# Optimization experiments

Hardware: AMD Instinct MI355X
Metric: run time of the kernel (lower is better)

## Reference

```python
import jax, jax.numpy as jnp
import numpy as np

T, D_IN, D_INT, D_OUT, B = 4096, 256, 256, 256, 8


def setup_inputs() -> dict:
    key = jax.random.key(0)
    ks = jax.random.split(key, 12)
    s_in = 1.0 / np.sqrt(D_IN)
    s_int = 1.0 / np.sqrt(D_INT)
    return {
        "x_batched": jax.random.normal(ks[0], (B, 1, T, D_IN), dtype=jnp.float32),
        "d_gamma_batched": jax.random.uniform(ks[1], (T, T), dtype=jnp.float32),
        "Wq": jax.random.uniform(ks[2], (D_IN, D_INT), jnp.float32, -s_in, s_in),
        "bq": jax.random.uniform(ks[3], (D_INT,), jnp.float32, -s_in, s_in),
        "Wk": jax.random.uniform(ks[4], (D_IN, D_INT), jnp.float32, -s_in, s_in),
        "bk": jax.random.uniform(ks[5], (D_INT,), jnp.float32, -s_in, s_in),
        "Wv": jax.random.uniform(ks[6], (D_IN, D_INT), jnp.float32, -s_in, s_in),
        "bv": jax.random.uniform(ks[7], (D_INT,), jnp.float32, -s_in, s_in),
        "Wo": jax.random.uniform(ks[8], (D_INT, D_OUT), jnp.float32, -s_int, s_int),
        "bo": jax.random.uniform(ks[9], (D_OUT,), jnp.float32, -s_int, s_int),
        "prelu_a": jnp.float32(0.25),  # PReLU single shared parameter, torch default init
    }


def reference(x_batched, d_gamma_batched, Wq, bq, Wk, bk, Wv, bv, Wo, bo, prelu_a):
    # x_batched: [B, 1, T, D_in] -> per-sample [T, D_in]
    x = x_batched.reshape(x_batched.shape[0], T, D_IN)  # [B, T, D_in]
    q = x @ Wq + bq  # [B, T, D_int]
    k = x @ Wk + bk
    v = x @ Wv + bv
    scores = jnp.einsum('btd,bsd->bts', q, k)  # [B, T, T] QK^T per sample
    retained = jnp.einsum('bts,bsd->btd', d_gamma_batched * scores, v)  # decay-gated, matmul V
    y = retained @ Wo + bo  # [B, T, D_out]
    out = jnp.where(y >= 0, y, prelu_a * y)  # PReLU
    return out  # [B, num_nodes=T, D_out]
```

## Files before the change

kernel.cpp:

```cpp
#include <hip/hip_runtime.h>

typedef unsigned short u16;
typedef __bf16 bf16x8 __attribute__((ext_vector_type(8)));
typedef float f32x4 __attribute__((ext_vector_type(4)));
typedef u16 u16x8 __attribute__((ext_vector_type(8)));

constexpr int T_DIM = 4096;
constexpr int DH    = 256;

__device__ __forceinline__ u16 f2bf(float f) {
    union { float f; unsigned u; } v; v.f = f;
    return (u16)((v.u + 0x7FFFu + ((v.u >> 16) & 1u)) >> 16);
}

__device__ __forceinline__ void gload_lds(const void* g, void* l) {
    __builtin_amdgcn_global_load_lds(
        (const __attribute__((address_space(1))) void*)g,
        (__attribute__((address_space(3))) void*)l, 16, 0, 0);
}

__global__ __launch_bounds__(256) void prep_w(
    const float* __restrict__ Wq, const float* __restrict__ Wk,
    const float* __restrict__ Wv, const float* __restrict__ Wo,
    u16* __restrict__ Wqt, u16* __restrict__ Wkt,
    u16* __restrict__ Wvt, u16* __restrict__ Wot)
{
    int idx = blockIdx.x * 256 + threadIdx.x;
    int j = idx >> 8, k = idx & 255;
    int s = k * 256 + j;
    Wqt[idx] = f2bf(Wq[s]);
    Wkt[idx] = f2bf(Wk[s]);
    Wvt[idx] = f2bf(Wv[s]);
    Wot[idx] = f2bf(Wo[s]);
}

__global__ __launch_bounds__(512, 2) void qkv_kernel(
    const float* __restrict__ x,
    const u16* __restrict__ Wqt, const u16* __restrict__ Wkt, const u16* __restrict__ Wvt,
    const float* __restrict__ bq, const float* __restrict__ bk, const float* __restrict__ bv,
    u16* __restrict__ Qg, u16* __restrict__ Kg, u16* __restrict__ Vtg)
{
    __shared__ __align__(16) char lds[131072];
    char* xl = lds;
    const int tid = threadIdx.x;
    const int w = tid >> 6, l = tid & 63;
    const int lr = l & 15, lh = l >> 4;
    const long row0 = (long)blockIdx.x * 128;
    const long bb   = row0 >> 12;
    const int  t0   = (int)(row0 & 4095);

    const u16*  Wt3[3] = { Wqt, Wkt, Wvt };
    const float* b3[3] = { bq, bk, bv };

    {
        char* wb = lds + 65536;
        const char* ws = (const char*)Wqt;
        #pragma unroll
        for (int i = 0; i < 4; ++i) {
            int off = tid * 16 + i * 8192;
            int roww = off >> 9, slot = (off >> 4) & 31;
            gload_lds(ws + roww * 512 + ((slot * 16) ^ ((roww & 7) << 4)), wb + off);
        }
    }
    #pragma unroll
    for (int i = 0; i < 8; ++i) {
        int sid = tid + i * 512;
        int row = sid >> 5, slot = sid & 31;
        const float* src = x + (row0 + row) * DH + slot * 8;
        float4 a  = *(const float4*)(src);
        float4 b2 = *(const float4*)(src + 4);
        u16x8 p;
        p[0] = f2bf(a.x);  p[1] = f2bf(a.y);  p[2] = f2bf(a.z);  p[3] = f2bf(a.w);
        p[4] = f2bf(b2.x); p[5] = f2bf(b2.y); p[6] = f2bf(b2.z); p[7] = f2bf(b2.w);
        *(u16x8*)(xl + row * 512 + ((slot * 16) ^ ((row & 7) << 4))) = p;
    }
    __syncthreads();

    bf16x8 af[8];
    const int arow = w * 16 + lr;
    #pragma unroll
    for (int ks = 0; ks < 8; ++ks)
        af[ks] = *(const bf16x8*)(xl + arow * 512 + ((ks * 64 + lh * 16) ^ ((arow & 7) << 4)));

    for (int p = 0; p < 12; ++p) {
        char* wb = lds + 65536 + (p & 1) * 32768;
        if (p < 11) {
            int pn = p + 1;
            const char* ws = (const char*)Wt3[pn >> 2] + (pn & 3) * 32768;
            char* wn = lds + 65536 + (pn & 1) * 32768;
            #pragma unroll
            for (int i = 0; i < 4; ++i) {
                int off = tid * 16 + i * 8192;
                int roww = off >> 9, slot = (off >> 4) & 31;
                gload_lds(ws + roww * 512 + ((slot * 16) ^ ((roww & 7) << 4)), wn + off);
            }
        }
        const int tgt = p >> 2, qtr = p & 3;
        f32x4 acc[4] = {};
        #pragma unroll
        for (int ks = 0; ks < 8; ++ks) {
            #pragma unroll
            for (int n = 0; n < 4; ++n) {
                int nl = n * 16 + lr;
                bf16x8 bf = *(const bf16x8*)(wb + nl * 512 + ((ks * 64 + lh * 16) ^ ((nl & 7) << 4)));
                acc[n] = __builtin_amdgcn_mfma_f32_16x16x32_bf16(af[ks], bf, acc[n], 0, 0, 0);
            }
        }
        const float* bias = b3[tgt];
        if (tgt < 2) {
            u16* dst = (tgt == 0) ? Qg : Kg;
            long grow = row0 + w * 16 + lh * 4;
            #pragma unroll
            for (int n = 0; n < 4; ++n) {
                int col = qtr * 64 + n * 16 + lr;
                float bbv = bias[col];
                #pragma unroll
                for (int r = 0; r < 4; ++r)
                    dst[(grow + r) * DH + col] = f2bf(acc[n][r] + bbv);
            }
        } else {
            #pragma unroll
            for (int n = 0; n < 4; ++n) {
                int d = qtr * 64 + n * 16 + lr;
                float bbv = bias[d];
                #pragma unroll
                for (int r = 0; r < 4; ++r) {
                    int t = w * 16 + lh * 4 + r;
                    *(u16*)(xl + d * 256 + ((t * 2) ^ ((d & 7) << 4))) = f2bf(acc[n][r] + bbv);
                }
            }
        }
        __syncthreads();
    }

    #pragma unroll
    for (int i = 0; i < 8; ++i) {
        int sid = tid + i * 512;
        int d = sid >> 4, slot = sid & 15;
        u16x8 v = *(const u16x8*)(xl + d * 256 + ((slot * 16) ^ ((d & 7) << 4)));
        *(u16x8*)((char*)Vtg + ((bb * DH + d) * T_DIM + t0) * 2 + slot * 16) = v;
    }
}

__global__ __launch_bounds__(512, 2) void retention_kernel(
    const u16* __restrict__ Qg, const u16* __restrict__ Kg, const u16* __restrict__ Vtg,
    const float* __restrict__ gamma, const u16* __restrict__ Wot,
    const float* __restrict__ bo, const float* __restrict__ pa,
    float* __restrict__ out)
{
    __shared__ __align__(16) char base[147456];
    char* pl = base + 131072;
    const int tid = threadIdx.x;
    const int w = tid >> 6, l = tid & 63;
    const int lr = l & 15, lh = l >> 4;
    const int wq = w >> 1, dh = w & 1;
    const int b  = blockIdx.x >> 5;
    const int q0 = (blockIdx.x & 31) * 128;

    const char* kgb = (const char*)(Kg + (long)b * T_DIM * DH);
    const char* vgb = (const char*)Vtg + (long)b * DH * T_DIM * 2;
    const float* gwave = gamma + (long)(q0 + wq * 32) * T_DIM + dh * 32;

    bf16x8 qf[2][8];
    #pragma unroll
    for (int rg = 0; rg < 2; ++rg) {
        const char* qb = (const char*)(Qg + ((long)b * T_DIM + q0 + wq * 32 + rg * 16 + lr) * DH);
        #pragma unroll
        for (int ks = 0; ks < 8; ++ks)
            qf[rg][ks] = *(const bf16x8*)(qb + ks * 64 + lh * 16);
    }

    f32x4 acc[2][8] = {};

    {
        char* kn = base;
        #pragma unroll
        for (int i = 0; i < 4; ++i) {
            int off = w * 4096 + i * 1024 + l * 16;
            int row = off >> 9, slot = (off >> 4) & 31;
            gload_lds(kgb + row * 512 + ((slot * 16) ^ ((row & 7) << 4)),
                      kn + w * 4096 + i * 1024);
        }
        char* vn = base + 32768;
        #pragma unroll
        for (int i = 0; i < 4; ++i) {
            int off = w * 4096 + i * 1024 + l * 16;
            int row = off >> 7, slot = (off >> 4) & 7;
            gload_lds(vgb + (long)row * (T_DIM * 2) + ((slot * 16) ^ ((row & 7) << 4)),
                      vn + w * 4096 + i * 1024);
        }
    }

    for (int it = 0; it < 64; ++it) {
        const int s0 = it * 64;
        char* kl = base + (it & 1) * 65536;
        char* vl = kl + 32768;

        float gv0[2][4], gv1[2][4];
        {
            const float* gp = gwave + s0;
            #pragma unroll
            for (int n = 0; n < 2; ++n)
                #pragma unroll
                for (int r = 0; r < 4; ++r) {
                    gv0[n][r] = gp[(long)(lh * 4 + r) * T_DIM + n * 16 + lr];
                    gv1[n][r] = gp[(long)(16 + lh * 4 + r) * T_DIM + n * 16 + lr];
                }
        }
        __builtin_amdgcn_sched_barrier(0);

        asm volatile("s_waitcnt vmcnt(16)" ::: "memory");
        __builtin_amdgcn_s_barrier();
        __builtin_amdgcn_sched_barrier(0);

        if (it < 63) {
            const char* kg = kgb + (long)(s0 + 64) * 512;
            char* kn = base + ((it + 1) & 1) * 65536;
            #pragma unroll
            for (int i = 0; i < 4; ++i) {
                int off = w * 4096 + i * 1024 + l * 16;
                int row = off >> 9, slot = (off >> 4) & 31;
                gload_lds(kg + row * 512 + ((slot * 16) ^ ((row & 7) << 4)),
                          kn + w * 4096 + i * 1024);
            }
            const char* vg = vgb + (long)(s0 + 64) * 2;
            char* vn = kn + 32768;
            #pragma unroll
            for (int i = 0; i < 4; ++i) {
                int off = w * 4096 + i * 1024 + l * 16;
                int row = off >> 7, slot = (off >> 4) & 7;
                gload_lds(vg + (long)row * (T_DIM * 2) + ((slot * 16) ^ ((row & 7) << 4)),
                          vn + w * 4096 + i * 1024);
            }
        }

        #pragma unroll
        for (int n = 0; n < 2; ++n) {
            f32x4 sa = {}, sb = {};
            const int srow = dh * 32 + n * 16 + lr;
            #pragma unroll
            for (int ks = 0; ks < 8; ++ks) {
                bf16x8 kf = *(const bf16x8*)(kl + srow * 512 + ((ks * 64 + lh * 16) ^ ((srow & 7) << 4)));
                sa = __builtin_amdgcn_mfma_f32_16x16x32_bf16(qf[0][ks], kf, sa, 0, 0, 0);
                sb = __builtin_amdgcn_mfma_f32_16x16x32_bf16(qf[1][ks], kf, sb, 0, 0, 0);
            }
            const int cb = (dh * 32 + n * 16 + lr) * 2;
            #pragma unroll
            for (int r = 0; r < 4; ++r) {
                int pr0 = wq * 32 + lh * 4 + r;
                int pr1 = pr0 + 16;
                *(__bf16*)(pl + pr0 * 128 + (cb ^ (((pr0 >> 1) & 7) << 4))) =
                    (__bf16)(gv0[n][r] * sa[r]);
                *(__bf16*)(pl + pr1 * 128 + (cb ^ (((pr1 >> 1) & 7) << 4))) =
                    (__bf16)(gv1[n][r] * sb[r]);
            }
        }

        __builtin_amdgcn_sched_barrier(0);
        asm volatile("s_waitcnt lgkmcnt(0)" ::: "memory");
        __builtin_amdgcn_s_barrier();
        __builtin_amdgcn_sched_barrier(0);

        bf16x8 pa2[2][2];
        #pragma unroll
        for (int rg = 0; rg < 2; ++rg)
            #pragma unroll
            for (int k2 = 0; k2 < 2; ++k2) {
                int prr = wq * 32 + rg * 16 + lr;
                pa2[rg][k2] = *(const bf16x8*)(pl + prr * 128 + ((k2 * 64 + lh * 16) ^ (((prr >> 1) & 7) << 4)));
            }
        #pragma unroll
        for (int n = 0; n < 8; ++n) {
            int vrow = dh * 128 + n * 16 + lr;
            #pragma unroll
            for (int k2 = 0; k2 < 2; ++k2) {
                bf16x8 bv = *(const bf16x8*)(vl + vrow * 128 + ((k2 * 64 + lh * 16) ^ ((vrow & 7) << 4)));
                acc[0][n] = __builtin_amdgcn_mfma_f32_16x16x32_bf16(pa2[0][k2], bv, acc[0][n], 0, 0, 0);
                acc[1][n] = __builtin_amdgcn_mfma_f32_16x16x32_bf16(pa2[1][k2], bv, acc[1][n], 0, 0, 0);
            }
        }
    }

    {
        #pragma unroll
        for (int rg = 0; rg < 2; ++rg)
            #pragma unroll
            for (int n = 0; n < 8; ++n) {
                int d2 = (dh * 128 + n * 16 + lr) * 2;
                #pragma unroll
                for (int r = 0; r < 4; ++r) {
                    int q = wq * 32 + rg * 16 + lh * 4 + r;
                    *(__bf16*)(base + q * 512 + (d2 ^ (((q >> 1) & 7) << 4))) =
                        (__bf16)acc[rg][n][r];
                }
            }
    }
    __syncthreads();
    {
        const int arow = w * 16 + lr;
        f32x4 acc2[16] = {};
        #pragma unroll
        for (int ks = 0; ks < 8; ++ks) {
            bf16x8 a = *(const bf16x8*)(base + arow * 512 +
                        ((ks * 64 + lh * 16) ^ (((arow >> 1) & 7) << 4)));
            #pragma unroll
            for (int n = 0; n < 16; ++n) {
                bf16x8 bf = *(const bf16x8*)(Wot + (n * 16 + lr) * DH + ks * 32 + lh * 8);
                acc2[n] = __builtin_amdgcn_mfma_f32_16x16x32_bf16(a, bf, acc2[n], 0, 0, 0);
            }
        }
        const float alpha = pa[0];
        long grow = (long)b * T_DIM + q0 + w * 16 + lh * 4;
        #pragma unroll
        for (int n = 0; n < 16; ++n) {
            int col = n * 16 + lr;
            float bb = bo[col];
            #pragma unroll
            for (int r = 0; r < 4; ++r) {
                float y = acc2[n][r] + bb;
                out[(grow + r) * DH + col] = (y >= 0.f) ? y : alpha * y;
            }
        }
    }
}

extern "C" void kernel_launch(void* const* d_in, const int* in_sizes, int n_in,
                              void* d_out, int out_size, void* d_ws, size_t ws_size,
                              hipStream_t stream)
{
    const float* x     = (const float*)d_in[0];
    const float* gamma = (const float*)d_in[1];
    const float* Wq = (const float*)d_in[2];
    const float* bq = (const float*)d_in[3];
    const float* Wk = (const float*)d_in[4];
    const float* bk = (const float*)d_in[5];
    const float* Wv = (const float*)d_in[6];
    const float* bv = (const float*)d_in[7];
    const float* Wo = (const float*)d_in[8];
    const float* bo = (const float*)d_in[9];
    const float* pa = (const float*)d_in[10];
    float* out = (float*)d_out;

    char* ws = (char*)d_ws;
    const long SZ = 16777216L;
    u16* Wqt = (u16*)(ws);
    u16* Wkt = (u16*)(ws + 131072);
    u16* Wvt = (u16*)(ws + 262144);
    u16* Wot = (u16*)(ws + 393216);
    u16* Qg  = (u16*)(ws + 524288);
    u16* Kg  = (u16*)(ws + 524288 + SZ);
    u16* Vtg = (u16*)(ws + 524288 + 2 * SZ);

    hipLaunchKernelGGL(prep_w, dim3(256), dim3(256), 0, stream,
                       Wq, Wk, Wv, Wo, Wqt, Wkt, Wvt, Wot);
    hipLaunchKernelGGL(qkv_kernel, dim3(256), dim3(512), 0, stream,
                       x, Wqt, Wkt, Wvt, bq, bk, bv, Qg, Kg, Vtg);
    hipLaunchKernelGGL(retention_kernel, dim3(256), dim3(512), 0, stream,
                       Qg, Kg, Vtg, gamma, Wot, bo, pa, out);
}
```

Before: 228.0 us.

## Load V fragments directly from global into registers instead of LDS staging

V tiles are no longer double-buffered through LDS. Each wave now loads its 16 bf16x8 V fragments straight from global memory into registers at the start of every iteration, and the LDS footprint drops from 144KB to 80KB. The intent is to cut LDS traffic and LDS capacity pressure. The change also wraps both MFMA phases in s_setprio to favour matrix issue. The cost is higher VGPR pressure and global-load latency that is exposed within the same iteration, since V is fetched without prefetch across iterations.

```diff
diff --git a/kernel.cpp b/kernel.cpp
--- a/kernel.cpp
+++ b/kernel.cpp
@@ -148,8 +148,8 @@
     const float* __restrict__ bo, const float* __restrict__ pa,
     float* __restrict__ out)
 {
-    __shared__ __align__(16) char base[147456];
-    char* pl = base + 131072;
+    __shared__ __align__(16) char base[81920];
+    char* pl = base + 65536;
     const int tid = threadIdx.x;
     const int w = tid >> 6, l = tid & 63;
     const int lr = l & 15, lh = l >> 4;
@@ -160,6 +160,7 @@
     const char* kgb = (const char*)(Kg + (long)b * T_DIM * DH);
     const char* vgb = (const char*)Vtg + (long)b * DH * T_DIM * 2;
     const float* gwave = gamma + (long)(q0 + wq * 32) * T_DIM + dh * 32;
+    const char* vrowb = vgb + (long)(dh * 128 + lr) * (T_DIM * 2) + lh * 16;
 
     bf16x8 qf[2][8];
     #pragma unroll
@@ -181,20 +182,11 @@
             gload_lds(kgb + row * 512 + ((slot * 16) ^ ((row & 7) << 4)),
                       kn + w * 4096 + i * 1024);
         }
-        char* vn = base + 32768;
-        #pragma unroll
-        for (int i = 0; i < 4; ++i) {
-            int off = w * 4096 + i * 1024 + l * 16;
-            int row = off >> 7, slot = (off >> 4) & 7;
-            gload_lds(vgb + (long)row * (T_DIM * 2) + ((slot * 16) ^ ((row & 7) << 4)),
-                      vn + w * 4096 + i * 1024);
-        }
     }
 
     for (int it = 0; it < 64; ++it) {
         const int s0 = it * 64;
-        char* kl = base + (it & 1) * 65536;
-        char* vl = kl + 32768;
+        char* kl = base + (it & 1) * 32768;
 
         float gv0[2][4], gv1[2][4];
         {
@@ -209,13 +201,24 @@
         }
         __builtin_amdgcn_sched_barrier(0);
 
-        asm volatile("s_waitcnt vmcnt(16)" ::: "memory");
+        bf16x8 vv[16];
+        {
+            const char* vp = vrowb + (long)s0 * 2;
+            #pragma unroll
+            for (int n = 0; n < 8; ++n)
+                #pragma unroll
+                for (int k2 = 0; k2 < 2; ++k2)
+                    vv[n * 2 + k2] = *(const bf16x8*)(vp + (long)(n * 16) * (T_DIM * 2) + k2 * 64);
+        }
+        __builtin_amdgcn_sched_barrier(0);
+
+        asm volatile("s_waitcnt vmcnt(32)" ::: "memory");
         __builtin_amdgcn_s_barrier();
         __builtin_amdgcn_sched_barrier(0);
 
         if (it < 63) {
             const char* kg = kgb + (long)(s0 + 64) * 512;
-            char* kn = base + ((it + 1) & 1) * 65536;
+            char* kn = base + ((it + 1) & 1) * 32768;
             #pragma unroll
             for (int i = 0; i < 4; ++i) {
                 int off = w * 4096 + i * 1024 + l * 16;
@@ -223,17 +226,9 @@
                 gload_lds(kg + row * 512 + ((slot * 16) ^ ((row & 7) << 4)),
                           kn + w * 4096 + i * 1024);
             }
-            const char* vg = vgb + (long)(s0 + 64) * 2;
-            char* vn = kn + 32768;
-            #pragma unroll
-            for (int i = 0; i < 4; ++i) {
-                int off = w * 4096 + i * 1024 + l * 16;
-                int row = off >> 7, slot = (off >> 4) & 7;
-                gload_lds(vg + (long)row * (T_DIM * 2) + ((slot * 16) ^ ((row & 7) << 4)),
-                          vn + w * 4096 + i * 1024);
-            }
-        }
-
+        }
+
+        __builtin_amdgcn_s_setprio(1);
         #pragma unroll
         for (int n = 0; n < 2; ++n) {
             f32x4 sa = {}, sb = {};
@@ -255,6 +250,7 @@
                     (__bf16)(gv1[n][r] * sb[r]);
             }
         }
+        __builtin_amdgcn_s_setprio(0);
 
         __builtin_amdgcn_sched_barrier(0);
         asm volatile("s_waitcnt lgkmcnt(0)" ::: "memory");
@@ -269,16 +265,16 @@
                 int prr = wq * 32 + rg * 16 + lr;
                 pa2[rg][k2] = *(const bf16x8*)(pl + prr * 128 + ((k2 * 64 + lh * 16) ^ (((prr >> 1) & 7) << 4)));
             }
+        __builtin_amdgcn_s_setprio(1);
         #pragma unroll
         for (int n = 0; n < 8; ++n) {
-            int vrow = dh * 128 + n * 16 + lr;
             #pragma unroll
             for (int k2 = 0; k2 < 2; ++k2) {
-                bf16x8 bv = *(const bf16x8*)(vl + vrow * 128 + ((k2 * 64 + lh * 16) ^ ((vrow & 7) << 4)));
-                acc[0][n] = __builtin_amdgcn_mfma_f32_16x16x32_bf16(pa2[0][k2], bv, acc[0][n], 0, 0, 0);
-                acc[1][n] = __builtin_amdgcn_mfma_f32_16x16x32_bf16(pa2[1][k2], bv, acc[1][n], 0, 0, 0);
-            }
-        }
+                acc[0][n] = __builtin_amdgcn_mfma_f32_16x16x32_bf16(pa2[0][k2], vv[n * 2 + k2], acc[0][n], 0, 0, 0);
+                acc[1][n] = __builtin_amdgcn_mfma_f32_16x16x32_bf16(pa2[1][k2], vv[n * 2 + k2], acc[1][n], 0, 0, 0);
+            }
+        }
+        __builtin_amdgcn_s_setprio(0);
     }
 
     {
```

Result: slower. 560.9 us (+146.0%).
